# Performance work log

Hardware: AMD Instinct MI355X
Metric: run time of the kernel (lower is better)

## Reference

```python
import jax, jax.numpy as jnp
import numpy as np

N_NODES = 50000
N_EDGES = 1600000
IN_DIM, HID_DIM, OUT_DIM, HEADS = 128, 128, 64, 8
NEG_SLOPE = 0.2
BN_EPS = 1e-5


def setup_inputs() -> dict:
    key = jax.random.key(0)
    ks = jax.random.split(key, 12)
    hpc = HID_DIM // HEADS  # per-head channels of layer 1
    return {
        "x": jax.random.normal(ks[0], (N_NODES, IN_DIM), jnp.float32),
        "edge_index": jax.random.randint(ks[1], (2, N_EDGES), 0, N_NODES, jnp.int64),
        "W1": jax.random.normal(ks[2], (IN_DIM, HEADS * hpc), jnp.float32) * 0.05,
        "a1_src": jax.random.normal(ks[3], (HEADS, hpc), jnp.float32) * 0.1,
        "a1_dst": jax.random.normal(ks[4], (HEADS, hpc), jnp.float32) * 0.1,
        "b1": jnp.zeros((HEADS * hpc,), jnp.float32),
        "bn_gamma": jnp.ones((HID_DIM,), jnp.float32),
        "bn_beta": jnp.zeros((HID_DIM,), jnp.float32),
        "W2": jax.random.normal(ks[5], (HID_DIM, OUT_DIM), jnp.float32) * 0.05,
        "a2_src": jax.random.normal(ks[6], (1, OUT_DIM), jnp.float32) * 0.1,
        "a2_dst": jax.random.normal(ks[7], (1, OUT_DIM), jnp.float32) * 0.1,
        "b2": jnp.zeros((OUT_DIM,), jnp.float32),
    }


def _gat_conv(x, src, dst, W, a_src, a_dst, bias, heads, n_nodes):
    # x: [N, Fin]; src/dst: [E'] (self-loops already appended)
    hpc = W.shape[1] // heads
    h = (x @ W).reshape(n_nodes, heads, hpc)                 # [N,H,C]
    alpha_s = jnp.einsum("nhc,hc->nh", h, a_src)             # [N,H]
    alpha_d = jnp.einsum("nhc,hc->nh", h, a_dst)
    e = alpha_s[src] + alpha_d[dst]                          # [E',H]
    e = jax.nn.leaky_relu(e, NEG_SLOPE)
    # segment softmax over destination neighborhoods
    m = jax.ops.segment_max(e, dst, num_segments=n_nodes)    # [N,H]
    m = jnp.where(jnp.isfinite(m), m, 0.0)
    ee = jnp.exp(e - m[dst])
    denom = jax.ops.segment_sum(ee, dst, num_segments=n_nodes)
    alpha = ee / (denom[dst] + 1e-16)                        # [E',H]
    msg = h[src] * alpha[:, :, None]                         # [E',H,C]
    out = jax.ops.segment_sum(msg, dst, num_segments=n_nodes)  # [N,H,C]
    return out.reshape(n_nodes, heads * hpc) + bias


def _batch_norm(x, gamma, beta):
    mu = jnp.mean(x, axis=0)
    var = jnp.var(x, axis=0)
    return gamma * (x - mu) * jax.lax.rsqrt(var + BN_EPS) + beta


def reference(x, edge_index, W1, a1_src, a1_dst, b1, bn_gamma, bn_beta, W2, a2_src, a2_dst, b2):
    n = x.shape[0]
    loops = jnp.arange(n, dtype=edge_index.dtype)
    src = jnp.concatenate([edge_index[0], loops])            # PyG add_self_loops
    dst = jnp.concatenate([edge_index[1], loops])
    h = _gat_conv(x, src, dst, W1, a1_src, a1_dst, b1, HEADS, n)
    h = _batch_norm(h, bn_gamma, bn_beta)
    h = jax.nn.elu(h)
    # dropout: identity at inference
    out = _gat_conv(h, src, dst, W2, a2_src, a2_dst, b2, 1, n)
    return out
```

## Files before the change

### kernel.cpp

```cpp
#include <hip/hip_runtime.h>
#include <hip/hip_bf16.h>

#define N_NODES 50000
#define N_EDGES 1600000
#define HEADS 8
#define NBK 196
#define NBLK 196
#define EPB 8192

typedef unsigned short u16;
typedef unsigned char u8;
typedef unsigned int u32;
typedef __attribute__((ext_vector_type(8))) short bf16x8;
typedef __attribute__((ext_vector_type(4))) float f32x4;

__device__ __forceinline__ float bf2f(u16 u) {
  union { u32 i; float f; } v; v.i = ((u32)u) << 16; return v.f;
}
__device__ __forceinline__ float bflo(u32 p) {
  union { u32 i; float f; } v; v.i = p << 16; return v.f;
}
__device__ __forceinline__ float bfhi(u32 p) {
  union { u32 i; float f; } v; v.i = p & 0xffff0000u; return v.f;
}
__device__ __forceinline__ u16 f2bf(float f) {
  union { float f; u32 i; } v; v.f = f;
  u32 r = v.i + 0x7fff + ((v.i >> 16) & 1);
  return (u16)(r >> 16);
}
__device__ __forceinline__ u32 pack2(float a, float b) {
  return (u32)f2bf(a) | ((u32)f2bf(b) << 16);
}
__device__ __forceinline__ int rfl(int x) { return __builtin_amdgcn_readfirstlane(x); }

__global__ void k_detect(const u16* __restrict__ x, const u32* __restrict__ ei,
                         int* __restrict__ flags) {
  __shared__ int cbig, cnz;
  if (threadIdx.x == 0) { cbig = 0; cnz = 0; }
  __syncthreads();
  int lb = 0, ln = 0;
  for (int i = threadIdx.x; i < 4096; i += 256) {
    int ex = (x[i] >> 7) & 0xff;
    lb += (ex >= 140);
    if (i < 2048) ln += (ei[2 * i + 1] != 0);
  }
  atomicAdd(&cbig, lb); atomicAdd(&cnz, ln);
  __syncthreads();
  if (threadIdx.x == 0) {
    flags[0] = (cbig > 16) ? 1 : 0;
    flags[1] = (cnz == 0) ? 1 : 0;
  }
}

__global__ void k_convsmall(const void* a1s, const void* a1d, const void* b1,
                            const void* gam, const void* bet, const void* a2s,
                            const void* a2d, const void* b2, const void* W1,
                            const void* W2, float* __restrict__ smallf,
                            u16* __restrict__ w1t, u16* __restrict__ w2t,
                            const int* __restrict__ flags) {
  int i = blockIdx.x * 256 + threadIdx.x;
  if (i >= 25408) return;
  bool f32 = flags[0] != 0;
  auto ld = [&](const void* p, int off) -> float {
    return f32 ? ((const float*)p)[off] : bf2f(((const u16*)p)[off]);
  };
  if (i >= 17216) {
    int j = i - 17216, n = j >> 7, k = j & 127;
    w2t[j] = f2bf(ld(W2, k * 64 + n));
  } else if (i >= 832) {
    int j = i - 832, n = j >> 7, k = j & 127;
    w1t[j] = f2bf(ld(W1, k * 128 + n));
  } else {
    const void* src; int off;
    if (i >= 768)      { src = b2;  off = i - 768; }
    else if (i >= 704) { src = a2d; off = i - 704; }
    else if (i >= 640) { src = a2s; off = i - 640; }
    else if (i >= 512) { src = bet; off = i - 512; }
    else if (i >= 384) { src = gam; off = i - 384; }
    else if (i >= 256) { src = b1;  off = i - 256; }
    else if (i >= 128) { src = a1d; off = i - 128; }
    else               { src = a1s; off = i; }
    smallf[i] = ld(src, off);
  }
}

__global__ __launch_bounds__(256) void k_hist(const int* __restrict__ ei,
                                              int* __restrict__ H,
                                              int* __restrict__ totals,
                                              const int* __restrict__ flags) {
  __shared__ int hist[NBK];
  int t = threadIdx.x, blk = blockIdx.x;
  for (int i = t; i < NBK; i += 256) hist[i] = 0;
  __syncthreads();
  bool i64 = flags[1] != 0;
  int base = blk * EPB;
  for (int k = 0; k < 32; k++) {
    int e = base + k * 256 + t;
    if (e < N_EDGES) {
      int d = i64 ? ei[2 * (N_EDGES + e)] : ei[N_EDGES + e];
      atomicAdd(&hist[d >> 8], 1);
    }
  }
  __syncthreads();
  for (int i = t; i < NBK; i += 256) {
    H[i * NBLK + blk] = hist[i];
    atomicAdd(&totals[i], hist[i]);
  }
}

__global__ void k_scan_blk(const int* __restrict__ H, const int* __restrict__ totals,
                           int* __restrict__ P) {
  __shared__ int tb[256], tmp[256];
  int t = threadIdx.x, b = blockIdx.x;
  int v0 = (t < NBK) ? totals[t] : 0;
  tb[t] = v0; __syncthreads();
  for (int o = 1; o < 256; o <<= 1) {
    int x = (t >= o) ? tb[t - o] : 0; __syncthreads();
    tb[t] += x; __syncthreads();
  }
  int base = (b == 0) ? 0 : tb[b - 1];
  int v = (t < NBLK) ? H[b * NBLK + t] : 0;
  tmp[t] = v; __syncthreads();
  for (int o = 1; o < 256; o <<= 1) {
    int x = (t >= o) ? tmp[t - o] : 0; __syncthreads();
    tmp[t] += x; __syncthreads();
  }
  if (t < NBLK) P[b * NBLK + t] = base + tmp[t] - v;
}

__global__ __launch_bounds__(256) void k_bucket(const int* __restrict__ ei,
                                                const int* __restrict__ P,
                                                u32* __restrict__ buf,
                                                const int* __restrict__ flags) {
  __shared__ u32 sv[EPB];
  __shared__ u16 rank[EPB];
  __shared__ u8  sk8[EPB];
  __shared__ int cnt[NBK], scn[NBK], tmp[256];
  int t = threadIdx.x, blk = blockIdx.x;
  int base = blk * EPB;
  int nE = N_EDGES - base; if (nE > EPB) nE = EPB;
  for (int i = t; i < NBK; i += 256) cnt[i] = 0;
  __syncthreads();
  bool i64 = flags[1] != 0;
  for (int k = 0; k < EPB / 256; k++) {
    int li = k * 256 + t, e = base + li;
    if (li < nE) {
      int d = i64 ? ei[2 * (N_EDGES + e)] : ei[N_EDGES + e];
      rank[li] = (u16)atomicAdd(&cnt[d >> 8], 1);
    }
  }
  __syncthreads();
  int v = (t < NBK) ? cnt[t] : 0;
  tmp[t] = v; __syncthreads();
  for (int o = 1; o < 256; o <<= 1) {
    int x = (t >= o) ? tmp[t - o] : 0; __syncthreads();
    tmp[t] += x; __syncthreads();
  }
  if (t < NBK) scn[t] = tmp[t] - v;
  __syncthreads();
  for (int k = 0; k < EPB / 256; k++) {
    int li = k * 256 + t, e = base + li;
    if (li < nE) {
      int s = i64 ? ei[2 * e] : ei[e];
      int d = i64 ? ei[2 * (N_EDGES + e)] : ei[N_EDGES + e];
      int key = d >> 8;
      int pos = scn[key] + rank[li];
      sv[pos] = ((u32)(d & 255) << 16) | (u32)s;
      sk8[pos] = (u8)key;
    }
  }
  __syncthreads();
  for (int i = t; i < nE; i += 256) {
    int b = sk8[i];
    buf[P[b * NBLK + blk] + (i - scn[b])] = sv[i];
  }
}

__global__ __launch_bounds__(256) void k_csr(const u32* __restrict__ buf,
                                             const int* __restrict__ totals,
                                             int* __restrict__ row_start,
                                             int* __restrict__ deg,
                                             int* __restrict__ csr, int N) {
  __shared__ int tb[256], cnt[256], scn[256], cur[256];
  int b = blockIdx.x, t = threadIdx.x;
  int v0 = (t < NBK) ? totals[t] : 0;
  tb[t] = v0; __syncthreads();
  for (int o = 1; o < 256; o <<= 1) {
    int x = (t >= o) ? tb[t - o] : 0; __syncthreads();
    tb[t] += x; __syncthreads();
  }
  int lo = (b == 0) ? 0 : tb[b - 1];
  int hi = tb[b];
  cnt[t] = 0; __syncthreads();
  for (int e = lo + t; e < hi; e += 256) atomicAdd(&cnt[(buf[e] >> 16) & 255], 1);
  __syncthreads();
  int v = cnt[t];
  scn[t] = v; __syncthreads();
  for (int o = 1; o < 256; o <<= 1) {
    int x = (t >= o) ? scn[t - o] : 0; __syncthreads();
    scn[t] += x; __syncthreads();
  }
  int excl = scn[t] - v;
  int node = b * 256 + t;
  if (node < N) { row_start[node] = lo + excl; deg[node] = v; }
  cur[t] = lo + excl;
  __syncthreads();
  for (int e = lo + t; e < hi; e += 256) {
    u32 p = buf[e];
    int pos = atomicAdd(&cur[(p >> 16) & 255], 1);
    csr[pos] = p & 0xffff;
  }
}

template <int NCOLS, bool EPI, bool ALPHA1, bool AFLAG>
__global__ __launch_bounds__(256) void k_gemm_mfma(const void* __restrict__ A,
                                                   const u16* __restrict__ BT,
                                                   const float* __restrict__ bnsum,
                                                   const float* __restrict__ bnsq,
                                                   const float* __restrict__ gamma,
                                                   const float* __restrict__ beta,
                                                   const float* __restrict__ va,
                                                   const float* __restrict__ vb,
                                                   float* __restrict__ as_out,
                                                   float* __restrict__ ad_out,
                                                   u16* __restrict__ C, int M,
                                                   const int* __restrict__ flags) {
  constexpr int KP = 136;
  constexpr int NT = NCOLS / 16;
  __shared__ u16 As[64 * KP];
  __shared__ u16 Bs[NCOLS * KP];
  __shared__ float sSc[128], sSh[128];
  int t = threadIdx.x;
  int row0 = blockIdx.x * 64;
  bool af32 = AFLAG ? (flags[0] != 0) : false;

  if (EPI) {
    if (t < 128) {
      float mu = bnsum[t] * (1.f / (float)N_NODES);
      float var = fmaxf(bnsq[t] * (1.f / (float)N_NODES) - mu * mu, 0.f);
      float sc = gamma[t] * rsqrtf(var + 1e-5f);
      sSc[t] = sc; sSh[t] = beta[t] - mu * sc;
    }
    __syncthreads();
  }

  for (int i = t; i < NCOLS * 16; i += 256) {
    int n = i >> 4, q = i & 15;
    *(uint4*)&Bs[n * KP + q * 8] = ((const uint4*)BT)[n * 16 + q];
  }
  for (int i = t; i < 64 * 32; i += 256) {
    int r = i >> 5, c4 = i & 31;
    int row = row0 + r;
    uint2 pk = make_uint2(0u, 0u);
    if (row < M) {
      if (EPI) {
        uint2 p = ((const uint2*)A)[(size_t)row * 32 + c4];
        int c = c4 * 4;
        float v0 = bflo(p.x), v1 = bfhi(p.x), v2 = bflo(p.y), v3 = bfhi(p.y);
        v0 = fmaf(v0, sSc[c],     sSh[c]);     v0 = v0 > 0.f ? v0 : __expf(v0) - 1.f;
        v1 = fmaf(v1, sSc[c + 1], sSh[c + 1]); v1 = v1 > 0.f ? v1 : __expf(v1) - 1.f;
        v2 = fmaf(v2, sSc[c + 2], sSh[c + 2]); v2 = v2 > 0.f ? v2 : __expf(v2) - 1.f;
        v3 = fmaf(v3, sSc[c + 3], sSh[c + 3]); v3 = v3 > 0.f ? v3 : __expf(v3) - 1.f;
        pk.x = pack2(v0, v1); pk.y = pack2(v2, v3);
      } else if (af32) {
        float4 v = ((const float4*)A)[(size_t)row * 32 + c4];
        pk.x = pack2(v.x, v.y); pk.y = pack2(v.z, v.w);
      } else {
        pk = ((const uint2*)A)[(size_t)row * 32 + c4];
      }
    }
    *(uint2*)&As[r * KP + c4 * 4] = pk;
  }
  __syncthreads();

  int lane = t & 63, w = t >> 6;
  int m = lane & 15, quad = lane >> 4;
  f32x4 acc[NT];
#pragma unroll
  for (int nt = 0; nt < NT; nt++) acc[nt] = (f32x4)(0.f);
  const u16* aBase = &As[(w * 16 + m) * KP + quad * 8];
  const u16* bBase = &Bs[m * KP + quad * 8];
#pragma unroll
  for (int ks = 0; ks < 4; ks++) {
    bf16x8 af = *(const bf16x8*)(aBase + ks * 32);
#pragma unroll
    for (int nt = 0; nt < NT; nt++) {
      bf16x8 bf = *(const bf16x8*)(bBase + nt * 16 * KP + ks * 32);
      acc[nt] = __builtin_amdgcn_mfma_f32_16x16x32_bf16(af, bf, acc[nt], 0, 0, 0);
    }
  }
  int orow0 = row0 + w * 16 + quad * 4;
#pragma unroll
  for (int nt = 0; nt < NT; nt++) {
#pragma unroll
    for (int r = 0; r < 4; r++) {
      int row = orow0 + r;
      if (row < M) C[(size_t)row * NCOLS + nt * 16 + m] = f2bf(acc[nt][r]);
    }
  }
  if (ALPHA1) {
    float pav[NT], pbv[NT];
#pragma unroll
    for (int nt = 0; nt < NT; nt++) { pav[nt] = va[nt * 16 + m]; pbv[nt] = vb[nt * 16 + m]; }
#pragma unroll
    for (int r = 0; r < 4; r++) {
      int row = orow0 + r;
#pragma unroll
      for (int nt = 0; nt < NT; nt++) {
        float vs = acc[nt][r] * pav[nt];
        float vd = acc[nt][r] * pbv[nt];
        vs += __shfl_xor(vs, 1); vd += __shfl_xor(vd, 1);
        vs += __shfl_xor(vs, 2); vd += __shfl_xor(vd, 2);
        vs += __shfl_xor(vs, 4); vd += __shfl_xor(vd, 4);
        vs += __shfl_xor(vs, 8); vd += __shfl_xor(vd, 8);
        if (row < M && m == 0) { as_out[row * 8 + nt] = vs; ad_out[row * 8 + nt] = vd; }
      }
    }
  }
  if (EPI) {
    float pav[NT], pbv[NT];
#pragma unroll
    for (int nt = 0; nt < NT; nt++) { pav[nt] = va[nt * 16 + m]; pbv[nt] = vb[nt * 16 + m]; }
#pragma unroll
    for (int r = 0; r < 4; r++) {
      float vs = 0.f, vd = 0.f;
#pragma unroll
      for (int nt = 0; nt < NT; nt++) {
        vs = fmaf(acc[nt][r], pav[nt], vs);
        vd = fmaf(acc[nt][r], pbv[nt], vd);
      }
      vs += __shfl_xor(vs, 1); vd += __shfl_xor(vd, 1);
      vs += __shfl_xor(vs, 2); vd += __shfl_xor(vd, 2);
      vs += __shfl_xor(vs, 4); vd += __shfl_xor(vd, 4);
      vs += __shfl_xor(vs, 8); vd += __shfl_xor(vd, 8);
      int row = orow0 + r;
      if (row < M && m == 0) { as_out[row] = vs; ad_out[row] = vd; }
    }
  }
}

__global__ __launch_bounds__(256) void k_agg1(const u16* __restrict__ h1b,
                                              const float* __restrict__ as_,
                                              const float* __restrict__ ad_,
                                              const int* __restrict__ csr,
                                              const int* __restrict__ row_start,
                                              const int* __restrict__ deg,
                                              const float* __restrict__ b1,
                                              u16* __restrict__ out, int N) {
  int node = blockIdx.x * 4 + (threadIdx.x >> 6);
  if (node >= N) return;
  int l = threadIdx.x & 63;
  int head = l >> 3, sub = l & 7;
  int eh = l >> 5, c2 = l & 31;
  int hch = c2 >> 2;
  int node_u = rfl(node);
  int st = rfl(row_start[node_u]);
  int cnt = rfl(deg[node_u]);
  const int* cp = csr + st;
  const uint2* h2p = (const uint2*)h1b;
  float ad = ad_[(node_u << 3) | head];
  float sp = 0.f, a0 = 0.f, a1 = 0.f, a2 = 0.f, a3 = 0.f;
  int j = 0;
  for (; j + 8 <= cnt; j += 8) {
    int ssub = cp[j + sub];
    float e = as_[(ssub << 3) | head] + ad;
    e = fmaxf(e, 0.2f * e);
    float p = __expf(e);
    sp += p;
#pragma unroll
    for (int k = 0; k < 4; k++) {
      int se = cp[j + 2 * k], so = cp[j + 2 * k + 1];
      int sk = eh ? so : se;
      float pk = __shfl(p, (hch << 3) | (2 * k + eh));
      uint2 hv = h2p[(size_t)sk * 32 + c2];
      a0 = fmaf(pk, bflo(hv.x), a0); a1 = fmaf(pk, bfhi(hv.x), a1);
      a2 = fmaf(pk, bflo(hv.y), a2); a3 = fmaf(pk, bfhi(hv.y), a3);
    }
  }
  for (; j <= cnt; j++) {
    int s0 = (j < cnt) ? rfl(cp[j]) : node_u;
    float e = as_[(s0 << 3) | head] + ad;
    e = fmaxf(e, 0.2f * e);
    float p = __expf(e);
    if (sub == 0) sp += p;
    float pk = __shfl(p, hch << 3);
    if (eh == 0) {
      uint2 hv = h2p[(size_t)s0 * 32 + c2];
      a0 = fmaf(pk, bflo(hv.x), a0); a1 = fmaf(pk, bfhi(hv.x), a1);
      a2 = fmaf(pk, bflo(hv.y), a2); a3 = fmaf(pk, bfhi(hv.y), a3);
    }
  }
  sp += __shfl_xor(sp, 1);
  sp += __shfl_xor(sp, 2);
  sp += __shfl_xor(sp, 4);
  float inv = 1.f / (__shfl(sp, hch << 3) + 1e-16f);
  a0 += __shfl_xor(a0, 32); a1 += __shfl_xor(a1, 32);
  a2 += __shfl_xor(a2, 32); a3 += __shfl_xor(a3, 32);
  if (eh == 0) {
    int c0 = c2 * 4;
    float r0 = fmaf(a0, inv, b1[c0]);
    float r1 = fmaf(a1, inv, b1[c0 + 1]);
    float r2 = fmaf(a2, inv, b1[c0 + 2]);
    float r3 = fmaf(a3, inv, b1[c0 + 3]);
    ((uint2*)out)[(size_t)node_u * 32 + c2] = make_uint2(pack2(r0, r1), pack2(r2, r3));
  }
}

__global__ void k_bnstat(const u16* __restrict__ h, float* __restrict__ gsum,
                         float* __restrict__ gsq, int N) {
  __shared__ float ts[256], tq[256];
  int t = threadIdx.x, col = t & 127, rr = t >> 7;
  int row0 = blockIdx.x * 128;
  float s = 0.f, q = 0.f;
  for (int r = rr; r < 128; r += 2) {
    int row = row0 + r;
    if (row < N) {
      float v = bf2f(h[((size_t)row << 7) + col]);
      s += v; q = fmaf(v, v, q);
    }
  }
  ts[t] = s; tq[t] = q; __syncthreads();
  if (t < 128) {
    atomicAdd(&gsum[t], ts[t] + ts[t + 128]);
    atomicAdd(&gsq[t], tq[t] + tq[t + 128]);
  }
}

__global__ __launch_bounds__(256) void k_agg2(const u16* __restrict__ h2b,
                                              const float* __restrict__ as_,
                                              const float* __restrict__ ad_,
                                              const int* __restrict__ csr,
                                              const int* __restrict__ row_start,
                                              const int* __restrict__ deg,
                                              const float* __restrict__ b2,
                                              void* __restrict__ out,
                                              const int* __restrict__ flags, int N) {
  int node = blockIdx.x * 4 + (threadIdx.x >> 6);
  if (node >= N) return;
  int l = threadIdx.x & 63;
  int sub = l & 7;
  int e4 = l >> 4, c4 = l & 15;
  int node_u = rfl(node);
  int st = rfl(row_start[node_u]);
  int cnt = rfl(deg[node_u]);
  const int* cp = csr + st;
  const uint2* h2p = (const uint2*)h2b;
  float ad = ad_[node_u];
  float sp = 0.f, a0 = 0.f, a1 = 0.f, a2 = 0.f, a3 = 0.f;
  int j = 0;
  for (; j + 8 <= cnt; j += 8) {
    int ssub = cp[j + sub];
    float e = as_[ssub] + ad;
    e = fmaxf(e, 0.2f * e);
    float p = __expf(e);
    if (l < 8) sp += p;
#pragma unroll
    for (int pass = 0; pass < 2; pass++) {
      int sa = cp[j + 4 * pass], sb = cp[j + 4 * pass + 1];
      int sc = cp[j + 4 * pass + 2], sd = cp[j + 4 * pass + 3];
      int sk = (e4 == 0) ? sa : (e4 == 1) ? sb : (e4 == 2) ? sc : sd;
      float pk = __shfl(p, 4 * pass + e4);
      uint2 hv = h2p[(size_t)sk * 16 + c4];
      a0 = fmaf(pk, bflo(hv.x), a0); a1 = fmaf(pk, bfhi(hv.x), a1);
      a2 = fmaf(pk, bflo(hv.y), a2); a3 = fmaf(pk, bfhi(hv.y), a3);
    }
  }
  for (; j <= cnt; j++) {
    int s0 = (j < cnt) ? rfl(cp[j]) : node_u;
    float e = as_[s0] + ad;
    e = fmaxf(e, 0.2f * e);
    float p = __expf(e);
    if (l == 0) sp += p;
    float pk = __shfl(p, 0);
    if (e4 == 0) {
      uint2 hv = h2p[(size_t)s0 * 16 + c4];
      a0 = fmaf(pk, bflo(hv.x), a0); a1 = fmaf(pk, bfhi(hv.x), a1);
      a2 = fmaf(pk, bflo(hv.y), a2); a3 = fmaf(pk, bfhi(hv.y), a3);
    }
  }
  sp += __shfl_xor(sp, 1);
  sp += __shfl_xor(sp, 2);
  sp += __shfl_xor(sp, 4);
  float inv = 1.f / (__shfl(sp, 0) + 1e-16f);
  a0 += __shfl_xor(a0, 16); a1 += __shfl_xor(a1, 16);
  a2 += __shfl_xor(a2, 16); a3 += __shfl_xor(a3, 16);
  a0 += __shfl_xor(a0, 32); a1 += __shfl_xor(a1, 32);
  a2 += __shfl_xor(a2, 32); a3 += __shfl_xor(a3, 32);
  if (e4 == 0) {
    int c0 = c4 * 4;
    float r0 = fmaf(a0, inv, b2[c0]);
    float r1 = fmaf(a1, inv, b2[c0 + 1]);
    float r2 = fmaf(a2, inv, b2[c0 + 2]);
    float r3 = fmaf(a3, inv, b2[c0 + 3]);
    if (flags[0]) {
      ((float4*)out)[(size_t)node_u * 16 + c4] = make_float4(r0, r1, r2, r3);
    } else {
      ((uint2*)out)[(size_t)node_u * 16 + c4] = make_uint2(pack2(r0, r1), pack2(r2, r3));
    }
  }
}

extern "C" void kernel_launch(void* const* d_in, const int* in_sizes, int n_in,
                              void* d_out, int out_size, void* d_ws, size_t ws_size,
                              hipStream_t stream) {
  const void* x   = d_in[0];
  const int*  ei  = (const int*)d_in[1];
  const void* W1  = d_in[2];
  const void* a1s = d_in[3];
  const void* a1d = d_in[4];
  const void* b1  = d_in[5];
  const void* gam = d_in[6];
  const void* bet = d_in[7];
  const void* W2  = d_in[8];
  const void* a2s = d_in[9];
  const void* a2d = d_in[10];
  const void* b2  = d_in[11];

  char* ws = (char*)d_ws;
  size_t off = 0;
  auto alloc = [&](size_t bytes) -> void* {
    void* p = ws + off;
    off += (bytes + 255) & ~(size_t)255;
    return p;
  };
  int* flags = (int*)alloc(256);
  char* zreg = (char*)alloc(2048);
  int* totals = (int*)zreg;
  float* gsum = (float*)(zreg + 1024);
  float* gsq  = gsum + 128;
  int* H  = (int*)alloc((size_t)NBK * NBLK * 4);
  int* P  = (int*)alloc((size_t)NBK * NBLK * 4);
  u32* ebuf = (u32*)alloc((size_t)N_EDGES * 4);
  int* csr = (int*)alloc((size_t)N_EDGES * 4);
  int* row_start = (int*)alloc((size_t)N_NODES * 4);
  int* deg = (int*)alloc((size_t)N_NODES * 4);
  float* smallf = (float*)alloc(832 * 4);
  float* a1sf = smallf;        float* a1df = smallf + 128;
  float* b1f  = smallf + 256;  float* gamf = smallf + 384;
  float* betf = smallf + 512;  float* a2sf = smallf + 640;
  float* a2df = smallf + 704;  float* b2f  = smallf + 768;
  u16* w1t = (u16*)alloc(16384 * 2);
  u16* w2t = (u16*)alloc(8192 * 2);
  u16* h1b  = (u16*)alloc((size_t)N_NODES * 128 * 2);
  u16* h1ob = (u16*)alloc((size_t)N_NODES * 128 * 2);
  u16* h2b  = (u16*)alloc((size_t)N_NODES * 64 * 2);
  float* al1s = (float*)alloc((size_t)N_NODES * 8 * 4);
  float* al1d = (float*)alloc((size_t)N_NODES * 8 * 4);
  float* al2s = (float*)alloc((size_t)N_NODES * 4);
  float* al2d = (float*)alloc((size_t)N_NODES * 4);
  if (off > ws_size) return;

  hipMemsetAsync(zreg, 0, 2048, stream);
  k_detect<<<1, 256, 0, stream>>>((const u16*)x, (const u32*)ei, flags);
  k_convsmall<<<100, 256, 0, stream>>>(a1s, a1d, b1, gam, bet, a2s, a2d, b2, W1, W2,
                                       smallf, w1t, w2t, flags);

  k_hist<<<NBLK, 256, 0, stream>>>(ei, H, totals, flags);
  k_scan_blk<<<NBK, 256, 0, stream>>>(H, totals, P);
  k_bucket<<<NBLK, 256, 0, stream>>>(ei, P, ebuf, flags);
  k_csr<<<NBK, 256, 0, stream>>>(ebuf, totals, row_start, deg, csr, N_NODES);

  k_gemm_mfma<128, false, true, true><<<(N_NODES + 63) / 64, 256, 0, stream>>>(
      x, w1t, nullptr, nullptr, nullptr, nullptr, a1sf, a1df, al1s, al1d,
      h1b, N_NODES, flags);
  k_agg1<<<(N_NODES + 3) / 4, 256, 0, stream>>>(h1b, al1s, al1d, csr, row_start, deg,
                                                b1f, h1ob, N_NODES);
  k_bnstat<<<(N_NODES + 127) / 128, 256, 0, stream>>>(h1ob, gsum, gsq, N_NODES);

  k_gemm_mfma<64, true, false, false><<<(N_NODES + 63) / 64, 256, 0, stream>>>(
      h1ob, w2t, gsum, gsq, gamf, betf, a2sf, a2df, al2s, al2d,
      h2b, N_NODES, flags);
  k_agg2<<<(N_NODES + 3) / 4, 256, 0, stream>>>(h2b, al2s, al2d, csr, row_start, deg,
                                                b2f, d_out, flags, N_NODES);
}
```

Baseline: 357.7 us.

## Remap aggregation lanes so each lane owns channels of every edge, dropping cross-half reductions

```diff
diff --git a/kernel.cpp b/kernel.cpp
--- a/kernel.cpp
+++ b/kernel.cpp
@@ -351,15 +351,14 @@
   if (node >= N) return;
   int l = threadIdx.x & 63;
   int head = l >> 3, sub = l & 7;
-  int eh = l >> 5, c2 = l & 31;
-  int hch = c2 >> 2;
+  int gbase = l & 56;
   int node_u = rfl(node);
   int st = rfl(row_start[node_u]);
   int cnt = rfl(deg[node_u]);
   const int* cp = csr + st;
-  const uint2* h2p = (const uint2*)h1b;
+  const u32* h32 = (const u32*)h1b;
   float ad = ad_[(node_u << 3) | head];
-  float sp = 0.f, a0 = 0.f, a1 = 0.f, a2 = 0.f, a3 = 0.f;
+  float sp = 0.f, a0 = 0.f, a1 = 0.f;
   int j = 0;
   for (; j + 8 <= cnt; j += 8) {
     int ssub = cp[j + sub];
@@ -368,42 +367,38 @@
     float p = __expf(e);
     sp += p;
 #pragma unroll
-    for (int k = 0; k < 4; k++) {
-      int se = cp[j + 2 * k], so = cp[j + 2 * k + 1];
-      int sk = eh ? so : se;
-      float pk = __shfl(p, (hch << 3) | (2 * k + eh));
-      uint2 hv = h2p[(size_t)sk * 32 + c2];
-      a0 = fmaf(pk, bflo(hv.x), a0); a1 = fmaf(pk, bfhi(hv.x), a1);
-      a2 = fmaf(pk, bflo(hv.y), a2); a3 = fmaf(pk, bfhi(hv.y), a3);
-    }
-  }
-  for (; j <= cnt; j++) {
-    int s0 = (j < cnt) ? rfl(cp[j]) : node_u;
-    float e = as_[(s0 << 3) | head] + ad;
-    e = fmaxf(e, 0.2f * e);
-    float p = __expf(e);
-    if (sub == 0) sp += p;
-    float pk = __shfl(p, hch << 3);
-    if (eh == 0) {
-      uint2 hv = h2p[(size_t)s0 * 32 + c2];
-      a0 = fmaf(pk, bflo(hv.x), a0); a1 = fmaf(pk, bfhi(hv.x), a1);
-      a2 = fmaf(pk, bflo(hv.y), a2); a3 = fmaf(pk, bfhi(hv.y), a3);
-    }
+    for (int k = 0; k < 8; k++) {
+      int sk = cp[j + k];
+      float pk = __shfl(p, gbase | k);
+      u32 hv = h32[(sk << 6) | l];
+      a0 = fmaf(pk, bflo(hv), a0);
+      a1 = fmaf(pk, bfhi(hv), a1);
+    }
+  }
+  for (; j < cnt; j++) {
+    int s0 = cp[j];
+    float e0 = as_[(s0 << 3) | head] + ad;
+    e0 = fmaxf(e0, 0.2f * e0);
+    float p0 = __expf(e0);
+    if (sub == 0) sp += p0;
+    u32 hv = h32[(s0 << 6) | l];
+    a0 = fmaf(p0, bflo(hv), a0); a1 = fmaf(p0, bfhi(hv), a1);
+  }
+  {
+    float e0 = as_[(node_u << 3) | head] + ad;
+    e0 = fmaxf(e0, 0.2f * e0);
+    float p0 = __expf(e0);
+    if (sub == 0) sp += p0;
+    u32 hv = h32[((size_t)node_u << 6) | l];
+    a0 = fmaf(p0, bflo(hv), a0); a1 = fmaf(p0, bfhi(hv), a1);
   }
   sp += __shfl_xor(sp, 1);
   sp += __shfl_xor(sp, 2);
   sp += __shfl_xor(sp, 4);
-  float inv = 1.f / (__shfl(sp, hch << 3) + 1e-16f);
-  a0 += __shfl_xor(a0, 32); a1 += __shfl_xor(a1, 32);
-  a2 += __shfl_xor(a2, 32); a3 += __shfl_xor(a3, 32);
-  if (eh == 0) {
-    int c0 = c2 * 4;
-    float r0 = fmaf(a0, inv, b1[c0]);
-    float r1 = fmaf(a1, inv, b1[c0 + 1]);
-    float r2 = fmaf(a2, inv, b1[c0 + 2]);
-    float r3 = fmaf(a3, inv, b1[c0 + 3]);
-    ((uint2*)out)[(size_t)node_u * 32 + c2] = make_uint2(pack2(r0, r1), pack2(r2, r3));
-  }
+  float inv = 1.f / (sp + 1e-16f);
+  int c0 = l * 2;
+  ((u32*)out)[((size_t)node_u << 6) + l] =
+      pack2(fmaf(a0, inv, b1[c0]), fmaf(a1, inv, b1[c0 + 1]));
 }
 
 __global__ void k_bnstat(const u16* __restrict__ h, float* __restrict__ gsum,
@@ -438,66 +433,49 @@
   int node = blockIdx.x * 4 + (threadIdx.x >> 6);
   if (node >= N) return;
   int l = threadIdx.x & 63;
-  int sub = l & 7;
-  int e4 = l >> 4, c4 = l & 15;
+  int sub = l & 7, gbase = l & 56;
   int node_u = rfl(node);
   int st = rfl(row_start[node_u]);
   int cnt = rfl(deg[node_u]);
   const int* cp = csr + st;
-  const uint2* h2p = (const uint2*)h2b;
   float ad = ad_[node_u];
-  float sp = 0.f, a0 = 0.f, a1 = 0.f, a2 = 0.f, a3 = 0.f;
+  float sp = 0.f, a = 0.f;
   int j = 0;
   for (; j + 8 <= cnt; j += 8) {
     int ssub = cp[j + sub];
     float e = as_[ssub] + ad;
     e = fmaxf(e, 0.2f * e);
     float p = __expf(e);
-    if (l < 8) sp += p;
-#pragma unroll
-    for (int pass = 0; pass < 2; pass++) {
-      int sa = cp[j + 4 * pass], sb = cp[j + 4 * pass + 1];
-      int sc = cp[j + 4 * pass + 2], sd = cp[j + 4 * pass + 3];
-      int sk = (e4 == 0) ? sa : (e4 == 1) ? sb : (e4 == 2) ? sc : sd;
-      float pk = __shfl(p, 4 * pass + e4);
-      uint2 hv = h2p[(size_t)sk * 16 + c4];
-      a0 = fmaf(pk, bflo(hv.x), a0); a1 = fmaf(pk, bfhi(hv.x), a1);
-      a2 = fmaf(pk, bflo(hv.y), a2); a3 = fmaf(pk, bfhi(hv.y), a3);
-    }
-  }
-  for (; j <= cnt; j++) {
-    int s0 = (j < cnt) ? rfl(cp[j]) : node_u;
-    float e = as_[s0] + ad;
-    e = fmaxf(e, 0.2f * e);
-    float p = __expf(e);
-    if (l == 0) sp += p;
-    float pk = __shfl(p, 0);
-    if (e4 == 0) {
-      uint2 hv = h2p[(size_t)s0 * 16 + c4];
-      a0 = fmaf(pk, bflo(hv.x), a0); a1 = fmaf(pk, bfhi(hv.x), a1);
-      a2 = fmaf(pk, bflo(hv.y), a2); a3 = fmaf(pk, bfhi(hv.y), a3);
-    }
+    sp += p;
+#pragma unroll
+    for (int k = 0; k < 8; k++) {
+      int sk = cp[j + k];
+      float pk = __shfl(p, gbase | k);
+      a = fmaf(pk, bf2f((h2b + (sk << 6))[l]), a);
+    }
+  }
+  for (; j < cnt; j++) {
+    int s0 = cp[j];
+    float e0 = as_[s0] + ad;
+    e0 = fmaxf(e0, 0.2f * e0);
+    float p0 = __expf(e0);
+    if (sub == 0) sp += p0;
+    a = fmaf(p0, bf2f((h2b + (s0 << 6))[l]), a);
+  }
+  {
+    float e0 = as_[node_u] + ad;
+    e0 = fmaxf(e0, 0.2f * e0);
+    float p0 = __expf(e0);
+    if (sub == 0) sp += p0;
+    a = fmaf(p0, bf2f((h2b + (node_u << 6))[l]), a);
   }
   sp += __shfl_xor(sp, 1);
   sp += __shfl_xor(sp, 2);
   sp += __shfl_xor(sp, 4);
-  float inv = 1.f / (__shfl(sp, 0) + 1e-16f);
-  a0 += __shfl_xor(a0, 16); a1 += __shfl_xor(a1, 16);
-  a2 += __shfl_xor(a2, 16); a3 += __shfl_xor(a3, 16);
-  a0 += __shfl_xor(a0, 32); a1 += __shfl_xor(a1, 32);
-  a2 += __shfl_xor(a2, 32); a3 += __shfl_xor(a3, 32);
-  if (e4 == 0) {
-    int c0 = c4 * 4;
-    float r0 = fmaf(a0, inv, b2[c0]);
-    float r1 = fmaf(a1, inv, b2[c0 + 1]);
-    float r2 = fmaf(a2, inv, b2[c0 + 2]);
-    float r3 = fmaf(a3, inv, b2[c0 + 3]);
-    if (flags[0]) {
-      ((float4*)out)[(size_t)node_u * 16 + c4] = make_float4(r0, r1, r2, r3);
-    } else {
-      ((uint2*)out)[(size_t)node_u * 16 + c4] = make_uint2(pack2(r0, r1), pack2(r2, r3));
-    }
-  }
+  float r = a / (sp + 1e-16f) + b2[l];
+  size_t idx = ((size_t)node_u << 6) + l;
+  if (flags[0]) ((float*)out)[idx] = r;
+  else          ((u16*)out)[idx] = f2bf(r);
 }
 
 extern "C" void kernel_launch(void* const* d_in, const int* in_sizes, int n_in,
```

Result: faster. 334.2 us (-6.6%).
